# Kernel optimization log

Measured on AMD Instinct MI355X. Metric: run time of the kernel, lower is better.

## Reference

```python
import jax, jax.numpy as jnp
import numpy as np

NUM_HEADS = 8  # config.num_heads


def setup_inputs() -> dict:
    key = jax.random.key(0)
    k0, k1, k2, k3, k4 = jax.random.split(key, 5)
    B, N, C, E = 32, 20000, 8, 512
    query_embeddings = jax.random.normal(k0, (B, E), dtype=jnp.float32)
    all_embeddings = jax.random.normal(k1, (N, E), dtype=jnp.float32)
    label_mask = jax.random.bernoulli(k2, 0.5, (N, C))  # bool multi-label mask
    # per-class MultiheadAttention q/k in-projection params (torch Linear convention: x @ W.T + b)
    Wq = jax.random.normal(k3, (C, E, E), dtype=jnp.float32) * 0.02
    Wk = jax.random.normal(k4, (C, E, E), dtype=jnp.float32) * 0.02
    bq = jnp.zeros((C, E), dtype=jnp.float32)
    bk = jnp.zeros((C, E), dtype=jnp.float32)
    return {
        "query_embeddings": query_embeddings,
        "all_embeddings": all_embeddings,
        "label_mask": label_mask,
        "Wq": Wq,
        "bq": bq,
        "Wk": Wk,
        "bk": bk,
        "n_samples": 5,
    }


def reference(query_embeddings, all_embeddings, label_mask, Wq, bq, Wk, bk, n_samples):
    """Vectorized-over-classes version of EmbeddingSelector.get_similar_samples.

    For each class c: q = query @ Wq[c].T + bq[c]; k_c over the class's database
    members; per-head scaled-dot softmax; attn weights averaged over heads
    (torch MHA need_weights default); top-k over class members. Non-members are
    masked to -inf before softmax, so they get weight 0 and (since every class
    has >> n_samples members) never enter the top-k -- identical math to the
    per-class gather loop, with global indices returned directly.
    """
    C, E, _ = Wq.shape
    H = NUM_HEADS
    dh = E // H
    B = query_embeddings.shape[0]
    N = all_embeddings.shape[0]

    # per-class projections (torch Linear: x @ W.T + b)
    q = jnp.einsum('be,cfe->cbf', query_embeddings, Wq) + bq[:, None, :]   # (C,B,E)
    k = jnp.einsum('ne,cfe->cnf', all_embeddings, Wk) + bk[:, None, :]     # (C,N,E)
    q = q.reshape(C, B, H, dh)
    k = k.reshape(C, N, H, dh)

    scale = 1.0 / jnp.sqrt(jnp.asarray(dh, q.dtype))
    scores = jnp.einsum('cbhd,cnhd->cbhn', q, k) * scale                   # (C,B,H,N)
    member = jnp.transpose(label_mask)[:, None, None, :]                   # (C,1,1,N)
    scores = jnp.where(member, scores, jnp.asarray(-1e9, scores.dtype))
    attn = jax.nn.softmax(scores, axis=-1).mean(axis=2)                    # (C,B,N) head-avg

    weights, indices = jax.lax.top_k(attn, n_samples)                      # (C,B,ns)
    result_weights = jnp.transpose(weights, (1, 0, 2))                     # (B,C,ns)
    result_indices = jnp.transpose(indices, (1, 0, 2)).astype(jnp.int32)   # (B,C,ns) global ids
    return result_indices, result_weights
```

## Files before the change

kernel.cpp:

```cpp
#include <hip/hip_runtime.h>
#include <math.h>

#define B_  32
#define N_  20000
#define C_  8
#define E_  512
#define H_  8
#define SCALE 0.125f
#define UNSC  9.765625e-4f

#define CHUNK 1024
#define NCH   20
#define NC3   157
#define NCG   20
#define SSZ ((size_t)B_ * H_ * N_)

typedef __attribute__((ext_vector_type(8))) _Float16 h8_t;
typedef __attribute__((ext_vector_type(8))) short   s8_t;
typedef __attribute__((ext_vector_type(4))) float f32x4;

#define MFMAH(a, b, c) __builtin_amdgcn_mfma_f32_16x16x32_f16(a, b, c, 0, 0, 0)

#define GLOAD_LDS16(g, l)                                              \
    __builtin_amdgcn_global_load_lds(                                  \
        (const __attribute__((address_space(1))) unsigned int*)(g),    \
        (__attribute__((address_space(3))) unsigned int*)(l), 16, 0, 0)

__device__ inline unsigned short f16_round(float x, float& fv) {
    _Float16 h = (_Float16)x;
    fv = (float)h;
    union { _Float16 hh; unsigned short us; } u;
    u.hh = h;
    return u.us;
}

__global__ __launch_bounds__(256) void k_q2(
        const float* __restrict__ x, const float* __restrict__ Wq,
        const float* __restrict__ bq, float* __restrict__ q) {
    int ft = blockIdx.x, c = blockIdx.y;
    int f0 = ft * 8;
    __shared__ float wsm[8][66];
    __shared__ float xs[32][66];
    int tid = threadIdx.x;
    int b = tid & 31, fs = tid >> 5;
    float acc = 0.f;
    const float* W = Wq + (size_t)c * E_ * E_;
    for (int k0 = 0; k0 < E_; k0 += 64) {
        __syncthreads();
        for (int i = tid; i < 512; i += 256)
            wsm[i >> 6][i & 63] = W[(size_t)(f0 + (i >> 6)) * E_ + k0 + (i & 63)];
        for (int i = tid; i < 2048; i += 256)
            xs[i >> 6][i & 63] = x[(size_t)(i >> 6) * E_ + k0 + (i & 63)];
        __syncthreads();
        #pragma unroll
        for (int kk = 0; kk < 64; ++kk)
            acc += xs[b][kk] * wsm[fs][kk];
    }
    q[((size_t)c * B_ + b) * E_ + f0 + fs] = acc + bq[c * E_ + f0 + fs];
}

#define U2P ((size_t)C_ * 16 * 16 * 512)

__global__ __launch_bounds__(256) void k_u2(
        const float* __restrict__ q, const float* __restrict__ Wk,
        const float* __restrict__ bk, short* __restrict__ u2,
        float* __restrict__ qb) {
    int et = blockIdx.x, h = blockIdx.y, c = blockIdx.z;
    int e0 = et * 64;
    __shared__ float qs[32][66];
    __shared__ float wk[64][66];
    int tid = threadIdx.x;
    int b = tid & 31, es = tid >> 5;
    for (int i = tid; i < 2048; i += 256)
        qs[i >> 6][i & 63] = q[((size_t)c * B_ + (i >> 6)) * E_ + h * 64 + (i & 63)];
    const float* W = Wk + (size_t)c * E_ * E_ + (size_t)(h * 64) * E_;
    for (int i = tid; i < 4096; i += 256)
        wk[i >> 6][i & 63] = W[(size_t)(i >> 6) * E_ + e0 + (i & 63)];
    __syncthreads();
    float acc[8] = {};
    for (int d = 0; d < 64; ++d) {
        float qv = qs[b][d];
        #pragma unroll
        for (int j = 0; j < 8; ++j)
            acc[j] += qv * wk[d][es * 8 + j];
    }
    int m   = b * 8 + h;
    int e0s = e0 + es * 8;
    int ks  = e0s >> 5, quad = (e0s & 31) >> 3;
    int lane = (m & 15) + 16 * quad;
    int mt  = m >> 4;
    size_t base = ((((size_t)c * 16 + mt) * 16 + ks) * 512) + (size_t)lane * 8;
    s8_t vh, vm;
    #pragma unroll
    for (int j = 0; j < 8; ++j) {
        float xv = acc[j] * 32.0f, fh, fm;
        vh[j] = (short)f16_round(xv, fh);
        vm[j] = (short)f16_round(xv - fh, fm);
    }
    *(s8_t*)(u2 + base)       = vh;
    *(s8_t*)(u2 + U2P + base) = vm;
    if (et == 0 && es == 0) {
        float s = 0.f;
        const float* bkr = bk + c * E_ + h * 64;
        for (int d = 0; d < 64; ++d) s += qs[b][d] * bkr[d];
        qb[c * 256 + b * 8 + h] = s;
    }
}

__global__ void k_split_A2(const float* __restrict__ A, short* __restrict__ A2t) {
    int nc = blockIdx.x, ks = blockIdx.y;
    int tid = threadIdx.x;
    int n = tid >> 1, kg = (tid & 1) * 2;
    int gn = nc * 128 + n;
    const float* ap = A + (size_t)gn * 512 + ks * 32 + kg * 8;
    s8_t vh[2], vm[2];
    #pragma unroll
    for (int g = 0; g < 2; ++g)
        #pragma unroll
        for (int j = 0; j < 8; ++j) {
            float x = (gn < N_) ? ap[g * 8 + j] * 32.0f : 0.f;
            float fh, fm;
            vh[g][j] = (short)f16_round(x, fh);
            vm[g][j] = (short)f16_round(x - fh, fm);
        }
    short* outp = A2t + ((size_t)nc * 16 + ks) * 8192 + n * 32;
    #pragma unroll
    for (int g = 0; g < 2; ++g) {
        int p = ((kg + g) + (n >> 1)) & 3;
        *(s8_t*)(outp + p * 8)        = vh[g];
        *(s8_t*)(outp + 4096 + p * 8) = vm[g];
    }
}

__global__ __launch_bounds__(256, 4) void k_scores_mfma(
        const short* __restrict__ u2, const short* __restrict__ A2t,
        const float* __restrict__ qb, const int* __restrict__ mask,
        float* __restrict__ S, float* __restrict__ Zpart, int c0, int CB) {
    __shared__ __align__(16) short As[16384];
    __shared__ float sQb[128];
    __shared__ int   sMask[128];
    int bx = blockIdx.x;
    int x     = bx & 7;
    int rest  = bx >> 3;
    int mh    = rest & 1;
    int rest2 = rest >> 1;
    int z     = rest2 % CB;
    int g     = rest2 / CB;
    int nc    = g * 8 + x;
    if (nc >= NC3) return;
    int c  = c0 + z;
    int tid = threadIdx.x;
    int lane = tid & 63, w = tid >> 6;
    int quad = lane >> 4, l15 = lane & 15;
    int n0 = nc * 128;

    if (tid < 128) {
        sQb[tid] = qb[c * 256 + mh * 128 + tid];
        int n = n0 + tid;
        sMask[tid] = (n < N_) ? mask[(size_t)n * C_ + c] : 0;
    }

    f32x4 acc[2][8];
    #pragma unroll
    for (int i = 0; i < 2; ++i)
        #pragma unroll
        for (int j = 0; j < 8; ++j)
            acc[i][j] = (f32x4){0.f, 0.f, 0.f, 0.f};

    const char* tb = (const char*)A2t + (size_t)nc * 262144;

    for (int ks2 = 0; ks2 < 8; ++ks2) {
        __syncthreads();
        const char* src = tb + (size_t)ks2 * 32768;
        #pragma unroll
        for (int t = 0; t < 8; ++t) {
            int seg = w * 8 + t;
            GLOAD_LDS16(src + (size_t)seg * 1024 + lane * 16,
                        (char*)As + seg * 1024);
        }
        __syncthreads();

        #pragma unroll
        for (int kh = 0; kh < 2; ++kh) {
            int ks = ks2 * 2 + kh;
            const short* Ab = As + kh * 8192;
            h8_t af[2][2];
            #pragma unroll
            for (int mt = 0; mt < 2; ++mt) {
                int mtg = mh * 8 + w * 2 + mt;
                size_t ub = ((((size_t)c * 16 + mtg) * 16 + ks) * 512)
                            + (size_t)lane * 8;
                af[mt][0] = *(const h8_t*)(u2 + ub);
                af[mt][1] = *(const h8_t*)(u2 + U2P + ub);
            }
            #pragma unroll
            for (int half = 0; half < 2; ++half) {
                __builtin_amdgcn_sched_barrier(0);
                #pragma unroll
                for (int q4 = 0; q4 < 4; ++q4) {
                    int nt = half * 4 + q4;
                    int r = nt * 16 + l15;
                    const short* bp = Ab + r * 32 + ((quad + (r >> 1)) & 3) * 8;
                    h8_t b0 = *(const h8_t*)bp;
                    h8_t b1 = *(const h8_t*)(bp + 4096);
                    #pragma unroll
                    for (int mt = 0; mt < 2; ++mt) {
                        f32x4 a = acc[mt][nt];
                        a = MFMAH(af[mt][0], b0, a);
                        a = MFMAH(af[mt][0], b1, a);
                        a = MFMAH(af[mt][1], b0, a);
                        acc[mt][nt] = a;
                    }
                }
            }
        }
    }

    float* Sc = S + (size_t)z * SSZ;
    #pragma unroll
    for (int mt = 0; mt < 2; ++mt) {
        float rs[4] = {0.f, 0.f, 0.f, 0.f};
        #pragma unroll
        for (int nt = 0; nt < 8; ++nt) {
            int nl = nt * 16 + l15;
            int n = n0 + nl;
            int mem = sMask[nl];
            #pragma unroll
            for (int r = 0; r < 4; ++r) {
                int ml = w * 32 + mt * 16 + quad * 4 + r;
                float sc = SCALE * (acc[mt][nt][r] * UNSC + sQb[ml]);
                float ev = mem ? __expf(sc) : 0.f;
                rs[r] += ev;
                if (n < N_) Sc[(size_t)(mh * 128 + ml) * N_ + n] = ev;
            }
        }
        #pragma unroll
        for (int r = 0; r < 4; ++r) {
            float v = rs[r];
            v += __shfl_xor(v, 1); v += __shfl_xor(v, 2);
            v += __shfl_xor(v, 4); v += __shfl_xor(v, 8);
            if (l15 == 0) {
                int ml = w * 32 + mt * 16 + quad * 4 + r;
                Zpart[((size_t)nc * C_ + c) * 256 + mh * 128 + ml] = v;
            }
        }
    }
}

__global__ void k_zsum(const float* __restrict__ Zpart, float* __restrict__ Z, int c0) {
    int c = c0 + blockIdx.x;
    int i = c * 256 + threadIdx.x;
    float s = 0.f;
    for (int nc = 0; nc < NC3; ++nc) s += Zpart[(size_t)nc * (C_ * 256) + i];
    Z[i] = s;
}

__global__ __launch_bounds__(256) void k_topk1(
        const float* __restrict__ S, const float* __restrict__ Z,
        float2* __restrict__ cand, int c0, int ns) {
    int b = blockIdx.y, z = blockIdx.z;
    int tid = threadIdx.x;
    int lane = tid & 63, w = tid >> 6;
    int chunk = blockIdx.x * 4 + w;
    const float* Sc = S + (size_t)z * SSZ;

    float zr[H_];
    #pragma unroll
    for (int h = 0; h < H_; ++h)
        zr[h] = 0.125f / Z[(c0 + z) * (B_ * H_) + b * H_ + h];

    int base = chunk * CHUNK + lane * 4;
    float va[16];
    #pragma unroll
    for (int s = 0; s < 16; ++s) va[s] = 0.f;
    bool ok[4];
    #pragma unroll
    for (int j = 0; j < 4; ++j) ok[j] = (base + j * 256) < N_;

    #pragma unroll
    for (int h = 0; h < H_; ++h) {
        const float* row = Sc + (size_t)(b * H_ + h) * N_;
        float wz = zr[h];
        #pragma unroll
        for (int j = 0; j < 4; ++j) {
            if (ok[j]) {
                const float4 sv = *(const float4*)&row[base + j * 256];
                va[j * 4 + 0] += sv.x * wz;
                va[j * 4 + 1] += sv.y * wz;
                va[j * 4 + 2] += sv.z * wz;
                va[j * 4 + 3] += sv.w * wz;
            }
        }
    }
    #pragma unroll
    for (int j = 0; j < 4; ++j)
        if (!ok[j]) {
            va[j * 4 + 0] = -1.f; va[j * 4 + 1] = -1.f;
            va[j * 4 + 2] = -1.f; va[j * 4 + 3] = -1.f;
        }

    float2* cp = cand + (((size_t)z * B_ + b) * NCH + chunk) * ns;
    for (int j = 0; j < ns; ++j) {
        float bv = va[0]; int bs = 0;
        #pragma unroll
        for (int s = 1; s < 16; ++s)
            if (va[s] > bv) { bv = va[s]; bs = s; }
        int bn = ok[bs >> 2] ? (base + ((bs >> 2) << 8) + (bs & 3)) : N_;
        #pragma unroll
        for (int off = 1; off < 64; off <<= 1) {
            float ov = __shfl_xor(bv, off, 64);
            int   on = __shfl_xor(bn, off, 64);
            if (ov > bv || (ov == bv && on < bn)) { bv = ov; bn = on; }
        }
        if (lane == 0) cp[j] = make_float2(bv, (float)bn);
        #pragma unroll
        for (int s = 0; s < 16; ++s) {
            int n_s = base + ((s >> 2) << 8) + (s & 3);
            if (n_s == bn) va[s] = -2.f;
        }
    }
}

__global__ __launch_bounds__(256) void k_topk2(
        const float2* __restrict__ cand, float* __restrict__ out, int c0, int ns) {
    int b = blockIdx.x, z = blockIdx.y;
    int c = c0 + z;
    int tid = threadIdx.x;
    int ncand = NCH * ns;
    const float2* cb = cand + ((size_t)z * B_ + b) * ncand;
    float v = -3.f; int ix = N_ + 1;
    if (tid < ncand) { float2 e = cb[tid]; v = e.x; ix = (int)e.y; }
    __shared__ float sv[256];
    __shared__ int   si[256];
    __shared__ int   win;
    for (int j = 0; j < ns; ++j) {
        sv[tid] = v; si[tid] = ix;
        __syncthreads();
        for (int w = 128; w >= 1; w >>= 1) {
            if (tid < w) {
                float v2 = sv[tid + w]; int i2 = si[tid + w];
                if (v2 > sv[tid] || (v2 == sv[tid] && i2 < si[tid])) {
                    sv[tid] = v2; si[tid] = i2;
                }
            }
            __syncthreads();
        }
        if (tid == 0) {
            out[((size_t)b * C_ + c) * ns + j] = (float)si[0];
            out[(size_t)B_ * C_ * ns + ((size_t)b * C_ + c) * ns + j] = sv[0];
            win = si[0];
        }
        __syncthreads();
        if (ix == win) v = -3.f;
        __syncthreads();
    }
}

extern "C" void kernel_launch(void* const* d_in, const int* in_sizes, int n_in,
                              void* d_out, int out_size, void* d_ws, size_t ws_size,
                              hipStream_t stream) {
    const float* x    = (const float*)d_in[0];
    const float* A    = (const float*)d_in[1];
    const int*   mask = (const int*)  d_in[2];
    const float* Wq   = (const float*)d_in[3];
    const float* bq   = (const float*)d_in[4];
    const float* Wk   = (const float*)d_in[5];
    const float* bk   = (const float*)d_in[6];
    float* out = (float*)d_out;

    int ns = out_size / (2 * B_ * C_);

    float* ws = (float*)d_ws;
    float* q     = ws;
    float* qb    = q     + (size_t)C_ * B_ * E_;
    float* Z     = qb    + (size_t)C_ * B_ * H_;
    float* Zpart = Z     + (size_t)C_ * B_ * H_;
    short* u2    = (short*)(Zpart + (size_t)NC3 * C_ * 256);
    short* A2t   = u2 + 2 * U2P;
    float* S     = (float*)(A2t + (size_t)NC3 * 16 * 8192);
    size_t fixedFloats = (size_t)(S - ws);

    size_t candFloats = (size_t)C_ * B_ * NCH * ns * 2;
    int CB = 8;
    while (CB > 1 &&
           (fixedFloats + (size_t)CB * SSZ + candFloats + 16) * 4 > ws_size)
        CB >>= 1;
    float2* cand = (float2*)(S + (size_t)CB * SSZ);

    k_q2<<<dim3(64, C_), 256, 0, stream>>>(x, Wq, bq, q);
    k_u2<<<dim3(8, H_, C_), 256, 0, stream>>>(q, Wk, bk, u2, qb);
    k_split_A2<<<dim3(NC3, 16), 256, 0, stream>>>(A, A2t);

    for (int c0 = 0; c0 < C_; c0 += CB) {
        k_scores_mfma<<<NCG * 2 * 8 * CB, 256, 0, stream>>>(u2, A2t, qb, mask, S, Zpart, c0, CB);
        k_zsum<<<CB, 256, 0, stream>>>(Zpart, Z, c0);
        k_topk1<<<dim3(NCH / 4, B_, CB), 256, 0, stream>>>(S, Z, cand, c0, ns);
        k_topk2<<<dim3(B_, CB), 256, 0, stream>>>(cand, out, c0, ns);
    }
}
```

Before: 365.6 us.

## Merge prep kernels, fold Z reduction into topk1, use wave-shuffle topk2

Combines the A split-conversion and q projection into one launch, removing a kernel boundary. The separate Z-sum kernel is dropped: each topk1 block now reduces the partial softmax denominators itself, redundantly per block. topk2 becomes a single 64-lane wave doing shuffle-based argmax instead of a shared-memory tree reduction with barriers. The goal is fewer launches and less synchronization, at the cost of repeated Zpart reads in topk1.

```diff
diff --git a/kernel.cpp b/kernel.cpp
--- a/kernel.cpp
+++ b/kernel.cpp
@@ -34,32 +34,59 @@
     return u.us;
 }
 
-__global__ __launch_bounds__(256) void k_q2(
+#define U2P ((size_t)C_ * 16 * 16 * 512)
+
+__global__ __launch_bounds__(256) void k_prep(
+        const float* __restrict__ A, short* __restrict__ A2t,
         const float* __restrict__ x, const float* __restrict__ Wq,
         const float* __restrict__ bq, float* __restrict__ q) {
-    int ft = blockIdx.x, c = blockIdx.y;
-    int f0 = ft * 8;
-    __shared__ float wsm[8][66];
-    __shared__ float xs[32][66];
+    int bid = blockIdx.x;
     int tid = threadIdx.x;
-    int b = tid & 31, fs = tid >> 5;
-    float acc = 0.f;
-    const float* W = Wq + (size_t)c * E_ * E_;
-    for (int k0 = 0; k0 < E_; k0 += 64) {
-        __syncthreads();
-        for (int i = tid; i < 512; i += 256)
-            wsm[i >> 6][i & 63] = W[(size_t)(f0 + (i >> 6)) * E_ + k0 + (i & 63)];
-        for (int i = tid; i < 2048; i += 256)
-            xs[i >> 6][i & 63] = x[(size_t)(i >> 6) * E_ + k0 + (i & 63)];
-        __syncthreads();
-        #pragma unroll
-        for (int kk = 0; kk < 64; ++kk)
-            acc += xs[b][kk] * wsm[fs][kk];
-    }
-    q[((size_t)c * B_ + b) * E_ + f0 + fs] = acc + bq[c * E_ + f0 + fs];
-}
-
-#define U2P ((size_t)C_ * 16 * 16 * 512)
+    if (bid < NC3 * 16) {
+        int nc = bid >> 4, ks = bid & 15;
+        int n = tid >> 1, kg = (tid & 1) * 2;
+        int gn = nc * 128 + n;
+        const float* ap = A + (size_t)gn * 512 + ks * 32 + kg * 8;
+        s8_t vh[2], vm[2];
+        #pragma unroll
+        for (int g = 0; g < 2; ++g)
+            #pragma unroll
+            for (int j = 0; j < 8; ++j) {
+                float xv = (gn < N_) ? ap[g * 8 + j] * 32.0f : 0.f;
+                float fh, fm;
+                vh[g][j] = (short)f16_round(xv, fh);
+                vm[g][j] = (short)f16_round(xv - fh, fm);
+            }
+        short* outp = A2t + ((size_t)nc * 16 + ks) * 8192 + n * 32;
+        #pragma unroll
+        for (int g = 0; g < 2; ++g) {
+            int p = ((kg + g) + (n >> 1)) & 3;
+            *(s8_t*)(outp + p * 8)        = vh[g];
+            *(s8_t*)(outp + 4096 + p * 8) = vm[g];
+        }
+    } else {
+        int r = bid - NC3 * 16;
+        int ft = r & 63, c = r >> 6;
+        int f0 = ft * 8;
+        __shared__ float wsm[8][66];
+        __shared__ float xs[32][66];
+        int b = tid & 31, fs = tid >> 5;
+        float acc = 0.f;
+        const float* W = Wq + (size_t)c * E_ * E_;
+        for (int k0 = 0; k0 < E_; k0 += 64) {
+            __syncthreads();
+            for (int i = tid; i < 512; i += 256)
+                wsm[i >> 6][i & 63] = W[(size_t)(f0 + (i >> 6)) * E_ + k0 + (i & 63)];
+            for (int i = tid; i < 2048; i += 256)
+                xs[i >> 6][i & 63] = x[(size_t)(i >> 6) * E_ + k0 + (i & 63)];
+            __syncthreads();
+            #pragma unroll
+            for (int kk = 0; kk < 64; ++kk)
+                acc += xs[b][kk] * wsm[fs][kk];
+        }
+        q[((size_t)c * B_ + b) * E_ + f0 + fs] = acc + bq[c * E_ + f0 + fs];
+    }
+}
 
 __global__ __launch_bounds__(256) void k_u2(
         const float* __restrict__ q, const float* __restrict__ Wk,
@@ -104,31 +131,6 @@
         const float* bkr = bk + c * E_ + h * 64;
         for (int d = 0; d < 64; ++d) s += qs[b][d] * bkr[d];
         qb[c * 256 + b * 8 + h] = s;
-    }
-}
-
-__global__ void k_split_A2(const float* __restrict__ A, short* __restrict__ A2t) {
-    int nc = blockIdx.x, ks = blockIdx.y;
-    int tid = threadIdx.x;
-    int n = tid >> 1, kg = (tid & 1) * 2;
-    int gn = nc * 128 + n;
-    const float* ap = A + (size_t)gn * 512 + ks * 32 + kg * 8;
-    s8_t vh[2], vm[2];
-    #pragma unroll
-    for (int g = 0; g < 2; ++g)
-        #pragma unroll
-        for (int j = 0; j < 8; ++j) {
-            float x = (gn < N_) ? ap[g * 8 + j] * 32.0f : 0.f;
-            float fh, fm;
-            vh[g][j] = (short)f16_round(x, fh);
-            vm[g][j] = (short)f16_round(x - fh, fm);
-        }
-    short* outp = A2t + ((size_t)nc * 16 + ks) * 8192 + n * 32;
-    #pragma unroll
-    for (int g = 0; g < 2; ++g) {
-        int p = ((kg + g) + (n >> 1)) & 3;
-        *(s8_t*)(outp + p * 8)        = vh[g];
-        *(s8_t*)(outp + 4096 + p * 8) = vm[g];
     }
 }
 
@@ -247,27 +249,26 @@
     }
 }
 
-__global__ void k_zsum(const float* __restrict__ Zpart, float* __restrict__ Z, int c0) {
-    int c = c0 + blockIdx.x;
-    int i = c * 256 + threadIdx.x;
-    float s = 0.f;
-    for (int nc = 0; nc < NC3; ++nc) s += Zpart[(size_t)nc * (C_ * 256) + i];
-    Z[i] = s;
-}
-
 __global__ __launch_bounds__(256) void k_topk1(
-        const float* __restrict__ S, const float* __restrict__ Z,
+        const float* __restrict__ S, const float* __restrict__ Zpart,
         float2* __restrict__ cand, int c0, int ns) {
     int b = blockIdx.y, z = blockIdx.z;
     int tid = threadIdx.x;
     int lane = tid & 63, w = tid >> 6;
     int chunk = blockIdx.x * 4 + w;
+    int c = c0 + z;
     const float* Sc = S + (size_t)z * SSZ;
 
+    float zrl = 0.f;
+    if (lane < H_) {
+        float s = 0.f;
+        const float* zp = Zpart + (size_t)c * 256 + b * 8 + lane;
+        for (int nc = 0; nc < NC3; ++nc) s += zp[(size_t)nc * (C_ * 256)];
+        zrl = 0.125f / s;
+    }
     float zr[H_];
     #pragma unroll
-    for (int h = 0; h < H_; ++h)
-        zr[h] = 0.125f / Z[(c0 + z) * (B_ * H_) + b * H_ + h];
+    for (int h = 0; h < H_; ++h) zr[h] = __shfl(zrl, h, 64);
 
     int base = chunk * CHUNK + lane * 4;
     float va[16];
@@ -321,38 +322,32 @@
     }
 }
 
-__global__ __launch_bounds__(256) void k_topk2(
+__global__ __launch_bounds__(64) void k_topk2(
         const float2* __restrict__ cand, float* __restrict__ out, int c0, int ns) {
     int b = blockIdx.x, z = blockIdx.y;
     int c = c0 + z;
-    int tid = threadIdx.x;
+    int lane = threadIdx.x;
     int ncand = NCH * ns;
     const float2* cb = cand + ((size_t)z * B_ + b) * ncand;
-    float v = -3.f; int ix = N_ + 1;
-    if (tid < ncand) { float2 e = cb[tid]; v = e.x; ix = (int)e.y; }
-    __shared__ float sv[256];
-    __shared__ int   si[256];
-    __shared__ int   win;
+    float v0 = -3.f, v1 = -3.f;
+    int   i0 = N_ + 1, i1 = N_ + 2;
+    if (lane < ncand)      { float2 e = cb[lane];      v0 = e.x; i0 = (int)e.y; }
+    if (lane + 64 < ncand) { float2 e = cb[lane + 64]; v1 = e.x; i1 = (int)e.y; }
     for (int j = 0; j < ns; ++j) {
-        sv[tid] = v; si[tid] = ix;
-        __syncthreads();
-        for (int w = 128; w >= 1; w >>= 1) {
-            if (tid < w) {
-                float v2 = sv[tid + w]; int i2 = si[tid + w];
-                if (v2 > sv[tid] || (v2 == sv[tid] && i2 < si[tid])) {
-                    sv[tid] = v2; si[tid] = i2;
-                }
-            }
-            __syncthreads();
-        }
-        if (tid == 0) {
-            out[((size_t)b * C_ + c) * ns + j] = (float)si[0];
-            out[(size_t)B_ * C_ * ns + ((size_t)b * C_ + c) * ns + j] = sv[0];
-            win = si[0];
-        }
-        __syncthreads();
-        if (ix == win) v = -3.f;
-        __syncthreads();
+        float bv = v0; int bn = i0;
+        if (v1 > bv || (v1 == bv && i1 < bn)) { bv = v1; bn = i1; }
+        #pragma unroll
+        for (int off = 1; off < 64; off <<= 1) {
+            float ov = __shfl_xor(bv, off, 64);
+            int   on = __shfl_xor(bn, off, 64);
+            if (ov > bv || (ov == bv && on < bn)) { bv = ov; bn = on; }
+        }
+        if (lane == 0) {
+            out[((size_t)b * C_ + c) * ns + j] = (float)bn;
+            out[(size_t)B_ * C_ * ns + ((size_t)b * C_ + c) * ns + j] = bv;
+        }
+        if (i0 == bn) v0 = -3.f;
+        if (i1 == bn) v1 = -3.f;
     }
 }
 
@@ -373,8 +368,7 @@
     float* ws = (float*)d_ws;
     float* q     = ws;
     float* qb    = q     + (size_t)C_ * B_ * E_;
-    float* Z     = qb    + (size_t)C_ * B_ * H_;
-    float* Zpart = Z     + (size_t)C_ * B_ * H_;
+    float* Zpart = qb    + (size_t)C_ * B_ * H_;
     short* u2    = (short*)(Zpart + (size_t)NC3 * C_ * 256);
     short* A2t   = u2 + 2 * U2P;
     float* S     = (float*)(A2t + (size_t)NC3 * 16 * 8192);
@@ -387,14 +381,12 @@
         CB >>= 1;
     float2* cand = (float2*)(S + (size_t)CB * SSZ);
 
-    k_q2<<<dim3(64, C_), 256, 0, stream>>>(x, Wq, bq, q);
+    k_prep<<<NC3 * 16 + 512, 256, 0, stream>>>(A, A2t, x, Wq, bq, q);
     k_u2<<<dim3(8, H_, C_), 256, 0, stream>>>(q, Wk, bk, u2, qb);
-    k_split_A2<<<dim3(NC3, 16), 256, 0, stream>>>(A, A2t);
 
     for (int c0 = 0; c0 < C_; c0 += CB) {
         k_scores_mfma<<<NCG * 2 * 8 * CB, 256, 0, stream>>>(u2, A2t, qb, mask, S, Zpart, c0, CB);
-        k_zsum<<<CB, 256, 0, stream>>>(Zpart, Z, c0);
-        k_topk1<<<dim3(NCH / 4, B_, CB), 256, 0, stream>>>(S, Z, cand, c0, ns);
-        k_topk2<<<dim3(B_, CB), 256, 0, stream>>>(cand, out, c0, ns);
-    }
-}
+        k_topk1<<<dim3(NCH / 4, B_, CB), 256, 0, stream>>>(S, Zpart, cand, c0, ns);
+        k_topk2<<<dim3(B_, CB), 64, 0, stream>>>(cand, out, c0, ns);
+    }
+}
```

Result: faster. 353.0 us (-3.5%).
